# Kernel optimization log

Hardware: AMD Instinct MI355X
Metric: run time of the kernel (lower is better)

The kernel has to match this reference:

```python
import jax, jax.numpy as jnp
import numpy as np

B, SY, SX, D = 16, 2048, 2048, 128

def setup_inputs() -> dict:
    key = jax.random.key(0)
    kx, ky = jax.random.split(key)
    input_x = jax.random.normal(kx, (B, SX, D), dtype=jnp.float32)
    input_y = jax.random.normal(ky, (B, SY, D), dtype=jnp.float32)
    return {"input_x": input_x, "input_y": input_y}

def reference(input_x, input_y):
    # attention_matrix: [B, SY, SX] = y @ x^T
    attention_matrix = jnp.einsum('byd,bxd->byx', input_y, input_x)
    # softmax over x-sequence (dim=2)
    attention_weight = jax.nn.softmax(attention_matrix, axis=2)
    # visual: mean of raw scores over y-sequence (dim=1) -> [B, SX]
    attention_visual = jnp.mean(attention_matrix, axis=1)
    # out: weighted sum of x then mean over y-sequence -> [B, D]
    attention_out = jnp.einsum('byx,bxd->byd', attention_weight, input_x)
    attention_out = jnp.mean(attention_out, axis=1)
    return (attention_visual, attention_out)
```

## Files before the change

### kernel.cpp

```cpp
#include <hip/hip_runtime.h>
#include <math.h>

constexpr int Bn = 16, SY = 2048, SX = 2048, Dd = 128;
constexpr int XT = 32;
constexpr int PIT = 72;
constexpr int PP = 40;
constexpr float INV_N = 1.0f / 2048.0f;
constexpr float SHIFT = 60.0f;
constexpr size_t NE = (size_t)Bn * SY * Dd;

using half8  = __attribute__((ext_vector_type(8))) _Float16;
using half4  = __attribute__((ext_vector_type(4))) _Float16;
using bs8    = __attribute__((ext_vector_type(8))) short;
using floatx4 = __attribute__((ext_vector_type(4))) float;

#define DPP_ROR(v, ctrl) __int_as_float(__builtin_amdgcn_update_dpp( \
    __float_as_int(v), __float_as_int(v), (ctrl), 0xf, 0xf, false))

__device__ __forceinline__ float rowsum16(float v) {
  v += DPP_ROR(v, 0x121);
  v += DPP_ROR(v, 0x122);
  v += DPP_ROR(v, 0x124);
  v += DPP_ROR(v, 0x128);
  return v;
}

__device__ __forceinline__ float sel4(const float* a, int q) {
  float r = a[0];
  r = (q == 1) ? a[1] : r;
  r = (q == 2) ? a[2] : r;
  r = (q == 3) ? a[3] : r;
  return r;
}

__device__ __forceinline__ void gld_lds16(const void* g, void* l) {
  __builtin_amdgcn_global_load_lds(
      (const __attribute__((address_space(1))) void*)g,
      (__attribute__((address_space(3))) void*)l, 16, 0, 0);
}

__device__ __forceinline__ unsigned short bf16_rtn(float v) {
  unsigned int u = __float_as_uint(v);
  return (unsigned short)((u + 0x7fff + ((u >> 16) & 1)) >> 16);
}

__global__ void xprep_kernel(const float* __restrict__ x,
                             _Float16* __restrict__ x16, unsigned short* __restrict__ xT16) {
  __shared__ unsigned short lt[128 * PIT];
  const int t = threadIdx.x;
  const int b = blockIdx.x >> 5, rb = blockIdx.x & 31;

  const float* xp = x + ((size_t)b * SX + rb * 64) * Dd;
  _Float16* x16p = x16 + ((size_t)b * SX + rb * 64) * Dd;
  #pragma unroll
  for (int it = 0; it < 8; ++it) {
    int tau = it * 256 + t;
    int row = tau >> 5, c4 = tau & 31;
    floatx4 f = *(const floatx4*)(xp + row * Dd + 4 * c4);
    half4 h;
    h[0]=(_Float16)f[0]; h[1]=(_Float16)f[1]; h[2]=(_Float16)f[2]; h[3]=(_Float16)f[3];
    *(half4*)(x16p + row * Dd + 4 * c4) = h;
    #pragma unroll
    for (int j = 0; j < 4; ++j) lt[(4 * c4 + j) * PIT + row] = bf16_rtn(f[j]);
  }
  __syncthreads();
  #pragma unroll
  for (int it = 0; it < 4; ++it) {
    int tau = it * 256 + t;
    int d = tau >> 3, g = tau & 7;
    *(ulonglong2*)(xT16 + (size_t)(b * Dd + d) * SX + rb * 64 + g * 8) =
        *(const ulonglong2*)&lt[d * PIT + g * 8];
  }
}

__launch_bounds__(256, 2)
__global__ void attn_kernel(const _Float16* __restrict__ x16,
                            const unsigned short* __restrict__ xT16,
                            const float* __restrict__ y,
                            float* __restrict__ out_ws, float* __restrict__ ysump) {
  __shared__ _Float16 xrm[2][2][32 * 128];
  __shared__ unsigned short xtp[2][2][128 * 32];
  __shared__ unsigned short Pw[4][32 * PP];
  __shared__ float ml_l[4][32];
  __shared__ float ysw[2][128];
  __shared__ float cbuf[4][128];

  const int t = threadIdx.x;
  const int w = t >> 6, lane = t & 63;
  const int n = lane & 15, q = lane >> 4;
  const int ygrp = w >> 1, chunk = w & 1;
  const int xcd = blockIdx.x & 7, kk = blockIdx.x >> 3;
  const int b = (xcd << 1) | (kk & 1);
  const int yblk = kk >> 1;
  const int y0 = yblk * 64;

  half8 afrag[2][4];
  {
    float yss[4][8];
    #pragma unroll
    for (int k = 0; k < 4; ++k)
      #pragma unroll
      for (int j = 0; j < 8; ++j) yss[k][j] = 0.f;
    #pragma unroll
    for (int s = 0; s < 2; ++s) {
      const float* yrow = y + (size_t)(b * SY + y0 + ygrp * 32 + s * 16 + n) * Dd;
      #pragma unroll
      for (int k = 0; k < 4; ++k) {
        floatx4 f0 = *(const floatx4*)(yrow + k * 32 + q * 8);
        floatx4 f1 = *(const floatx4*)(yrow + k * 32 + q * 8 + 4);
        half8 h;
        h[0]=(_Float16)f0[0]; h[1]=(_Float16)f0[1]; h[2]=(_Float16)f0[2]; h[3]=(_Float16)f0[3];
        h[4]=(_Float16)f1[0]; h[5]=(_Float16)f1[1]; h[6]=(_Float16)f1[2]; h[7]=(_Float16)f1[3];
        afrag[s][k] = h;
        #pragma unroll
        for (int j = 0; j < 4; ++j) { yss[k][j] += f0[j]; yss[k][4 + j] += f1[j]; }
      }
    }
    #pragma unroll
    for (int k = 0; k < 4; ++k)
      #pragma unroll
      for (int j = 0; j < 8; ++j) {
        float v = rowsum16(yss[k][j]);
        if (chunk == 0 && n == 0) ysw[ygrp][k * 32 + q * 8 + j] = v;
      }
  }

  floatx4 acc_o[2][8];
  float lpart[2][4];
  #pragma unroll
  for (int s = 0; s < 2; ++s) {
    #pragma unroll
    for (int d = 0; d < 8; ++d) acc_o[s][d] = (floatx4){0, 0, 0, 0};
    #pragma unroll
    for (int r = 0; r < 4; ++r) lpart[s][r] = 0.f;
  }
  const floatx4 initS = (floatx4){-SHIFT, -SHIFT, -SHIFT, -SHIFT};

  const _Float16* xb = x16 + (size_t)b * SX * Dd;
  const unsigned short* xTb = xT16 + (size_t)b * Dd * SX;
  unsigned short* P = Pw[w];

  const int RL = w >> 1, RC = w & 1;
  int l_off[8];
  size_t boff[8];
  #pragma unroll
  for (int ii = 0; ii < 8; ++ii) {
    int G = ii * 64 + lane;
    l_off[ii] = G * 16;
    if (RL == 0) { int row = G >> 4, g = ((G & 15) - row) & 15;
                   boff[ii] = ((size_t)row * 128 + g * 8) * 2; }
    else         { int row = G >> 2, g = ((G & 3) - (row >> 2)) & 3;
                   boff[ii] = ((size_t)row * SX + g * 8) * 2; }
  }
  const char* gbase = RL ? (const char*)(xTb + (size_t)RC * 1024)
                         : (const char*)(xb + (size_t)RC * 1024 * 128);
  const size_t gstep = (RL ? (size_t)XT : (size_t)XT * 128) * 2;
  char* lbase = RL ? (char*)&xtp[RC][0][0] : (char*)&xrm[RC][0][0];

  #pragma unroll
  for (int ii = 0; ii < 8; ++ii)
    gld_lds16(gbase + boff[ii], lbase + l_off[ii]);
  __syncthreads();

  for (int it = 0; it < 32; ++it) {
    const int cur = it & 1;

    if (it + 1 < 32) {
      const char* gp = gbase + (size_t)(it + 1) * gstep;
      char* lp = lbase + (cur ^ 1) * 8192;
      #pragma unroll
      for (int ii = 0; ii < 8; ++ii)
        gld_lds16(gp + boff[ii], lp + l_off[ii]);
    }

    floatx4 sA[2][2];
    #pragma unroll
    for (int s = 0; s < 2; ++s) { sA[s][0] = initS; sA[s][1] = initS; }
    #pragma unroll
    for (int k = 0; k < 4; ++k) {
      half8 bf[2];
      #pragma unroll
      for (int c = 0; c < 2; ++c) {
        int row = 16 * c + n;
        int sw = (k * 4 + q + row) & 15;
        bf[c] = *(const half8*)&xrm[chunk][cur][row * 128 + sw * 8];
      }
      #pragma unroll
      for (int s = 0; s < 2; ++s)
        #pragma unroll
        for (int c = 0; c < 2; ++c)
          sA[s][c] = __builtin_amdgcn_mfma_f32_16x16x32_f16(afrag[s][k], bf[c], sA[s][c], 0, 0, 0);
    }

    #pragma unroll
    for (int s = 0; s < 2; ++s)
      #pragma unroll
      for (int r = 0; r < 4; ++r) {
        float e0 = __expf(sA[s][0][r]);
        float e1 = __expf(sA[s][1][r]);
        lpart[s][r] += e0 + e1;
        P[(s * 16 + 4 * q + r) * PP + n]      = bf16_rtn(e0);
        P[(s * 16 + 4 * q + r) * PP + 16 + n] = bf16_rtn(e1);
      }

    bs8 pf[2];
    #pragma unroll
    for (int s = 0; s < 2; ++s)
      pf[s] = *(const bs8*)&P[(s * 16 + n) * PP + q * 8];
    #pragma unroll
    for (int d = 0; d < 8; ++d) {
      int row = 16 * d + n;
      int sw = (q + (row >> 2)) & 3;
      bs8 xf = *(const bs8*)&xtp[chunk][cur][row * 32 + sw * 8];
      #pragma unroll
      for (int s = 0; s < 2; ++s)
        acc_o[s][d] = __builtin_amdgcn_mfma_f32_16x16x32_bf16(pf[s], xf, acc_o[s][d], 0, 0, 0);
    }

    __syncthreads();
  }

  float lrow[2][4];
  #pragma unroll
  for (int s = 0; s < 2; ++s)
    #pragma unroll
    for (int r = 0; r < 4; ++r) lrow[s][r] = rowsum16(lpart[s][r]);
  if (n == 0) {
    #pragma unroll
    for (int s = 0; s < 2; ++s)
      #pragma unroll
      for (int r = 0; r < 4; ++r) ml_l[w][s * 16 + 4 * q + r] = lrow[s][r];
  }
  __syncthreads();
  const int p = w ^ 1;
  float scale[2][4];
  #pragma unroll
  for (int s = 0; s < 2; ++s)
    #pragma unroll
    for (int r = 0; r < 4; ++r)
      scale[s][r] = 1.f / (lrow[s][r] + ml_l[p][s * 16 + 4 * q + r]);

  float ps[8];
  #pragma unroll
  for (int d = 0; d < 8; ++d) {
    float v = 0.f;
    #pragma unroll
    for (int s = 0; s < 2; ++s)
      #pragma unroll
      for (int r = 0; r < 4; ++r) v += scale[s][r] * acc_o[s][d][r];
    v += __shfl_xor(v, 16);
    v += __shfl_xor(v, 32);
    ps[d] = v;
  }
  cbuf[w][16 * q + n]      = sel4(ps, q);
  cbuf[w][64 + 16 * q + n] = sel4(ps + 4, q);
  __syncthreads();
  if (t < 128) {
    float s = cbuf[0][t] + cbuf[1][t] + cbuf[2][t] + cbuf[3][t];
    out_ws[(size_t)(b * 32 + yblk) * 128 + t] = s;
    ysump[(size_t)(b * 32 + yblk) * 128 + t] = ysw[0][t] + ysw[1][t];
  }
}

__global__ void finale_kernel(const _Float16* __restrict__ x16, const float* __restrict__ ysump,
                              const float* __restrict__ out_ws,
                              float* __restrict__ visual, float* __restrict__ out) {
  const int t = threadIdx.x, blk = blockIdx.x;
  if (blk < 128) {
    __shared__ float ysum[128];
    const int b = blk >> 3, x0 = (blk & 7) * 256;
    if (t < 128) {
      float s = 0.f;
      #pragma unroll
      for (int j = 0; j < 32; ++j) s += ysump[(size_t)(b * 32 + j) * 128 + t];
      ysum[t] = s;
    }
    __syncthreads();
    const int x = x0 + t;
    const _Float16* xr = x16 + ((size_t)b * SX + x) * Dd;
    float dot = 0.f;
    #pragma unroll
    for (int g = 0; g < 16; ++g) {
      half8 h = *(const half8*)(xr + g * 8);
      #pragma unroll
      for (int j = 0; j < 8; ++j) dot += ysum[g * 8 + j] * (float)h[j];
    }
    visual[(size_t)b * SX + x] = dot * INV_N;
  } else {
    #pragma unroll
    for (int i = 0; i < 8; ++i) {
      int e = i * 256 + t;
      int bb = e >> 7, d = e & 127;
      float s = 0.f;
      for (int j = 0; j < 32; ++j) s += out_ws[(size_t)(bb * 32 + j) * 128 + d];
      out[bb * 128 + d] = s * INV_N;
    }
  }
}

extern "C" void kernel_launch(void* const* d_in, const int* in_sizes, int n_in,
                              void* d_out, int out_size, void* d_ws, size_t ws_size,
                              hipStream_t stream) {
  const float* x = (const float*)d_in[0];
  const float* y = (const float*)d_in[1];
  float* visual = (float*)d_out;
  float* out    = (float*)d_out + (size_t)Bn * SX;

  _Float16* x16        = (_Float16*)d_ws;
  unsigned short* xT16 = (unsigned short*)(x16 + NE);
  float* wsf    = (float*)(xT16 + NE);
  float* out_ws = wsf;
  float* ysump  = wsf + (size_t)512 * 128;

  xprep_kernel<<<512, 256, 0, stream>>>(x, x16, xT16);
  attn_kernel<<<512, 256, 0, stream>>>(x16, xT16, y, out_ws, ysump);
  finale_kernel<<<129, 256, 0, stream>>>(x16, ysump, out_ws, visual, out);
}
```

Baseline: 135.3 us.

## Fold finale reduction into attention kernel via last-block atomic counter

Removes the separate finale kernel launch. Each attention block atomically increments a per-batch counter, and the last block for each batch reduces ysump and out_ws, then computes the visual dot products and the output mean. The xprep kernel also now does the fp16 copy with wider vector stores and builds the transposed bf16 tile with coalesced column reads and 64-bit LDS writes, using a new pitch. The cost is that 16 tail blocks, each running 256 threads, do the visual work serially over 2048 columns, which may lengthen the tail compared with a 128-block finale.

```diff
diff --git a/kernel.cpp b/kernel.cpp
--- a/kernel.cpp
+++ b/kernel.cpp
@@ -3,7 +3,7 @@
 
 constexpr int Bn = 16, SY = 2048, SX = 2048, Dd = 128;
 constexpr int XT = 32;
-constexpr int PIT = 72;
+constexpr int TP = 66;
 constexpr int PP = 40;
 constexpr float INV_N = 1.0f / 2048.0f;
 constexpr float SHIFT = 60.0f;
@@ -45,31 +45,47 @@
 }
 
 __global__ void xprep_kernel(const float* __restrict__ x,
-                             _Float16* __restrict__ x16, unsigned short* __restrict__ xT16) {
-  __shared__ unsigned short lt[128 * PIT];
+                             _Float16* __restrict__ x16, unsigned short* __restrict__ xT16,
+                             unsigned int* __restrict__ cnt) {
+  __shared__ unsigned short lt[128 * TP];
   const int t = threadIdx.x;
   const int b = blockIdx.x >> 5, rb = blockIdx.x & 31;
+  if (blockIdx.x == 0 && t < 16) cnt[t] = 0;
 
   const float* xp = x + ((size_t)b * SX + rb * 64) * Dd;
   _Float16* x16p = x16 + ((size_t)b * SX + rb * 64) * Dd;
+
+  #pragma unroll
+  for (int it = 0; it < 4; ++it) {
+    int tau = it * 256 + t;
+    int row = tau >> 4, c8 = tau & 15;
+    floatx4 f0 = *(const floatx4*)(xp + row * Dd + c8 * 8);
+    floatx4 f1 = *(const floatx4*)(xp + row * Dd + c8 * 8 + 4);
+    half8 h;
+    h[0]=(_Float16)f0[0]; h[1]=(_Float16)f0[1]; h[2]=(_Float16)f0[2]; h[3]=(_Float16)f0[3];
+    h[4]=(_Float16)f1[0]; h[5]=(_Float16)f1[1]; h[6]=(_Float16)f1[2]; h[7]=(_Float16)f1[3];
+    *(half8*)(x16p + row * Dd + c8 * 8) = h;
+  }
+
   #pragma unroll
   for (int it = 0; it < 8; ++it) {
     int tau = it * 256 + t;
-    int row = tau >> 5, c4 = tau & 31;
-    floatx4 f = *(const floatx4*)(xp + row * Dd + 4 * c4);
-    half4 h;
-    h[0]=(_Float16)f[0]; h[1]=(_Float16)f[1]; h[2]=(_Float16)f[2]; h[3]=(_Float16)f[3];
-    *(half4*)(x16p + row * Dd + 4 * c4) = h;
-    #pragma unroll
-    for (int j = 0; j < 4; ++j) lt[(4 * c4 + j) * PIT + row] = bf16_rtn(f[j]);
-  }
-  __syncthreads();
+    int d = tau & 127, rg = tau >> 7;
+    unsigned short v[4];
+    #pragma unroll
+    for (int j = 0; j < 4; ++j) v[j] = bf16_rtn(xp[(rg * 4 + j) * Dd + d]);
+    *(ulonglong1*)&lt[d * TP + rg * 4] =
+        (ulonglong1){ (unsigned long long)v[0] | ((unsigned long long)v[1] << 16) |
+                      ((unsigned long long)v[2] << 32) | ((unsigned long long)v[3] << 48) };
+  }
+  __syncthreads();
+
   #pragma unroll
   for (int it = 0; it < 4; ++it) {
     int tau = it * 256 + t;
     int d = tau >> 3, g = tau & 7;
     *(ulonglong2*)(xT16 + (size_t)(b * Dd + d) * SX + rb * 64 + g * 8) =
-        *(const ulonglong2*)&lt[d * PIT + g * 8];
+        *(const ulonglong2*)&lt[d * TP + g * 8];
   }
 }
 
@@ -77,13 +93,17 @@
 __global__ void attn_kernel(const _Float16* __restrict__ x16,
                             const unsigned short* __restrict__ xT16,
                             const float* __restrict__ y,
-                            float* __restrict__ out_ws, float* __restrict__ ysump) {
+                            float* __restrict__ out_ws, float* __restrict__ ysump,
+                            float* __restrict__ visual, float* __restrict__ out,
+                            unsigned int* __restrict__ cnt) {
   __shared__ _Float16 xrm[2][2][32 * 128];
   __shared__ unsigned short xtp[2][2][128 * 32];
   __shared__ unsigned short Pw[4][32 * PP];
   __shared__ float ml_l[4][32];
   __shared__ float ysw[2][128];
   __shared__ float cbuf[4][128];
+  __shared__ float ysumS[128];
+  __shared__ unsigned int aold_s;
 
   const int t = threadIdx.x;
   const int w = t >> 6, lane = t & 63;
@@ -260,40 +280,38 @@
     out_ws[(size_t)(b * 32 + yblk) * 128 + t] = s;
     ysump[(size_t)(b * 32 + yblk) * 128 + t] = ysw[0][t] + ysw[1][t];
   }
-}
-
-__global__ void finale_kernel(const _Float16* __restrict__ x16, const float* __restrict__ ysump,
-                              const float* __restrict__ out_ws,
-                              float* __restrict__ visual, float* __restrict__ out) {
-  const int t = threadIdx.x, blk = blockIdx.x;
-  if (blk < 128) {
-    __shared__ float ysum[128];
-    const int b = blk >> 3, x0 = (blk & 7) * 256;
+  __threadfence();
+  __syncthreads();
+  if (t == 0) aold_s = atomicAdd(cnt + b, 1u);
+  __syncthreads();
+
+  if (aold_s == 31u) {
+    __threadfence();
     if (t < 128) {
       float s = 0.f;
       #pragma unroll
       for (int j = 0; j < 32; ++j) s += ysump[(size_t)(b * 32 + j) * 128 + t];
-      ysum[t] = s;
+      ysumS[t] = s;
     }
     __syncthreads();
-    const int x = x0 + t;
-    const _Float16* xr = x16 + ((size_t)b * SX + x) * Dd;
-    float dot = 0.f;
-    #pragma unroll
-    for (int g = 0; g < 16; ++g) {
-      half8 h = *(const half8*)(xr + g * 8);
-      #pragma unroll
-      for (int j = 0; j < 8; ++j) dot += ysum[g * 8 + j] * (float)h[j];
-    }
-    visual[(size_t)b * SX + x] = dot * INV_N;
-  } else {
-    #pragma unroll
-    for (int i = 0; i < 8; ++i) {
-      int e = i * 256 + t;
-      int bb = e >> 7, d = e & 127;
+    #pragma unroll
+    for (int c = 0; c < 8; ++c) {
+      const int xcol = c * 256 + t;
+      const _Float16* xr = x16 + ((size_t)b * SX + xcol) * Dd;
+      float dot = 0.f;
+      #pragma unroll
+      for (int g = 0; g < 16; ++g) {
+        half8 h = *(const half8*)(xr + g * 8);
+        #pragma unroll
+        for (int j = 0; j < 8; ++j) dot += ysumS[g * 8 + j] * (float)h[j];
+      }
+      visual[(size_t)b * SX + xcol] = dot * INV_N;
+    }
+    if (t < 128) {
       float s = 0.f;
-      for (int j = 0; j < 32; ++j) s += out_ws[(size_t)(bb * 32 + j) * 128 + d];
-      out[bb * 128 + d] = s * INV_N;
+      #pragma unroll
+      for (int j = 0; j < 32; ++j) s += out_ws[(size_t)(b * 32 + j) * 128 + t];
+      out[b * 128 + t] = s * INV_N;
     }
   }
 }
@@ -311,8 +329,8 @@
   float* wsf    = (float*)(xT16 + NE);
   float* out_ws = wsf;
   float* ysump  = wsf + (size_t)512 * 128;
-
-  xprep_kernel<<<512, 256, 0, stream>>>(x, x16, xT16);
-  attn_kernel<<<512, 256, 0, stream>>>(x16, xT16, y, out_ws, ysump);
-  finale_kernel<<<129, 256, 0, stream>>>(x16, ysump, out_ws, visual, out);
-}
+  unsigned int* cnt = (unsigned int*)(ysump + (size_t)512 * 128);
+
+  xprep_kernel<<<512, 256, 0, stream>>>(x, x16, xT16, cnt);
+  attn_kernel<<<512, 256, 0, stream>>>(x16, xT16, y, out_ws, ysump, visual, out, cnt);
+}
```

After: 182.0 us. 1.35x slower.
